# Kernel tuning notes

Measured on AMD Instinct MI355X. Metric: run time of the kernel, lower is better.

The kernel has to match this reference:

```python
import jax, jax.numpy as jnp
import numpy as np
from functools import partial

H = 768
E = 1536
B = 4
L = 4096

def layer_norm(x, g, b, eps=1e-5):
    mu = jnp.mean(x, axis=-1, keepdims=True)
    var = jnp.mean((x - mu) ** 2, axis=-1, keepdims=True)
    return (x - mu) * jax.lax.rsqrt(var + eps) * g + b

def l2_normalize(x, eps=1e-12):
    n = jnp.sqrt(jnp.sum(x * x, axis=-1, keepdims=True))
    return x / jnp.maximum(n, eps)

def dw_conv(x, w):
    # x: [B, L, E], w: [E, 1, 3] depthwise kernel (torch Conv1d groups=E layout)
    y = jax.lax.conv_general_dilated(
        x.transpose(0, 2, 1), w, window_strides=(1,), padding=[(1, 1)],
        dimension_numbers=('NCH', 'OIH', 'NCH'), feature_group_count=E)
    return y.transpose(0, 2, 1)

def setup_inputs() -> dict:
    key = jax.random.key(0)
    ks = jax.random.split(key, 12)
    d = {}
    d['x'] = jax.random.normal(ks[0], (B, L, H), jnp.float32)
    d['ln1_g'] = jnp.ones((H,), jnp.float32)
    d['ln1_b'] = jnp.zeros((H,), jnp.float32)
    d['ln2_g'] = jnp.ones((E,), jnp.float32)
    d['ln2_b'] = jnp.zeros((E,), jnp.float32)
    d['W_in'] = 0.02 * jax.random.normal(ks[1], (3 * E, H), jnp.float32)
    d['b_in'] = jnp.zeros((3 * E,), jnp.float32)
    d['W_beta'] = jnp.zeros((E, H), jnp.float32)  # torch init: constant 0
    d['b_beta'] = jnp.ones((E,), jnp.float32)     # torch init: constant 1
    d['W_out'] = 0.02 * jax.random.normal(ks[2], (H, E), jnp.float32)
    d['b_out'] = jnp.zeros((H,), jnp.float32)
    d['W1'] = 0.02 * jax.random.normal(ks[3], (4 * H, H), jnp.float32)
    d['b1'] = jnp.zeros((4 * H,), jnp.float32)
    d['W2'] = 0.02 * jax.random.normal(ks[4], (H, 4 * H), jnp.float32)
    d['b2'] = jnp.zeros((H,), jnp.float32)
    d['conv_w'] = jax.random.normal(ks[5], (E, 1, 3), jnp.float32) / jnp.sqrt(3.0)
    d['attn_scale'] = jnp.ones((1,), jnp.float32)
    return d

def reference(x, ln1_g, ln1_b, ln2_g, ln2_b, W_in, b_in, W_beta, b_beta,
              W_out, b_out, W1, b1, W2, b2, conv_w, attn_scale):
    shortcut = x
    xn = layer_norm(x, ln1_g, ln1_b)
    qkv = xn @ W_in.T + b_in
    q, k, v = jnp.split(qkv, 3, axis=-1)
    q = jax.nn.silu(q)
    k = jax.nn.silu(k)
    v = jax.nn.gelu(v, approximate=False)
    q = l2_normalize(q) + 0.1 * k
    k = l2_normalize(k) + 0.1 * q
    q = dw_conv(q, conv_w)
    k = dw_conv(k, conv_w)
    v = dw_conv(v, conv_w)
    beta = jax.nn.sigmoid(xn @ W_beta.T + b_beta) * 0.9 + 0.1
    # initial state is zero, so v_old = 0 and v_new = beta * v (same math as torch code)
    v_new = beta * v                                   # [B, L, E]
    state = jnp.einsum('ble,blf->bef', v_new, k)       # v_new^T @ k : [B, E, E]
    out = jnp.einsum('blf,bef->ble', q, state)         # q @ state^T
    out = out * attn_scale
    out = layer_norm(out, ln2_g, ln2_b)
    out = out @ W_out.T + b_out
    x = shortcut + out
    h = layer_norm(x, ln1_g, ln1_b)
    h = jax.nn.gelu(h @ W1.T + b1, approximate=False) @ W2.T + b2
    return x + h
```

## Files before the change

kernel.cpp:

```cpp
#include <hip/hip_runtime.h>
#include <hip/hip_bf16.h>
#include <cstdint>
#include <cstddef>

using bf16_t = __hip_bfloat16;
typedef __bf16 bf16x8 __attribute__((ext_vector_type(8)));
typedef float f32x4 __attribute__((ext_vector_type(4)));

#define DEVI static __device__ __forceinline__

DEVI float b2f(bf16_t v) { return __bfloat162float(v); }
DEVI bf16_t f2b(float v) { return __float2bfloat16(v); }

DEVI float fsigmoid(float x) { return 1.0f / (1.0f + __expf(-x)); }
DEVI float fsilu(float x) { return x * fsigmoid(x); }
DEVI float fgelu(float x) { return 0.5f * x * (1.0f + erff(x * 0.70710678118654752440f)); }

DEVI void g2l16(const bf16_t* g, bf16_t* l) {
    __builtin_amdgcn_global_load_lds(
        (const __attribute__((address_space(1))) void*)g,
        (__attribute__((address_space(3))) void*)l,
        16, 0, 0);
}

template<int ACT, bool RESID, bool OUTBF, bool QKVSPLIT>
__global__ __launch_bounds__(256) void gemm_nt(
    const bf16_t* __restrict__ A, const bf16_t* __restrict__ B,
    void* __restrict__ Cout, const float* __restrict__ bias,
    const float* __restrict__ resid,
    int M, int N, int K, long long sA, long long sB, long long sC)
{
    __shared__ bf16_t As[128 * 32];
    __shared__ bf16_t Bs[128 * 32];

    const int t  = threadIdx.x;
    const int w  = t >> 6;
    const int ln = t & 63;
    const long long bz = blockIdx.z;
    A += bz * sA;
    B += bz * sB;
    const long long cbase = QKVSPLIT ? 0 : bz * sC;

    const int m0 = blockIdx.y * 128;
    const int n0 = blockIdx.x * 128;
    const int wm = (w >> 1) * 64;
    const int wn = (w & 1) * 64;

    f32x4 acc[4][4] = {};

    const int rI0 = (w * 2 + 0) * 16 + (ln >> 2);
    const int rI1 = (w * 2 + 1) * 16 + (ln >> 2);
    const int kc8 = (ln & 3) * 8;
    bf16_t* ldsA0 = &As[(w * 2 + 0) * 512];
    bf16_t* ldsA1 = &As[(w * 2 + 1) * 512];
    bf16_t* ldsB0 = &Bs[(w * 2 + 0) * 512];
    bf16_t* ldsB1 = &Bs[(w * 2 + 1) * 512];

    const int q8 = (ln >> 4) * 8;
    const int fr = ln & 15;

    for (int k0 = 0; k0 < K; k0 += 32) {
        g2l16(A + (size_t)(m0 + rI0) * K + k0 + kc8, ldsA0);
        g2l16(A + (size_t)(m0 + rI1) * K + k0 + kc8, ldsA1);
        g2l16(B + (size_t)(n0 + rI0) * K + k0 + kc8, ldsB0);
        g2l16(B + (size_t)(n0 + rI1) * K + k0 + kc8, ldsB1);
        __syncthreads();

        bf16x8 af[4], bfr[4];
#pragma unroll
        for (int i = 0; i < 4; ++i) {
            af[i]  = *(const bf16x8*)&As[(wm + i * 16 + fr) * 32 + q8];
            bfr[i] = *(const bf16x8*)&Bs[(wn + i * 16 + fr) * 32 + q8];
        }
#pragma unroll
        for (int mi = 0; mi < 4; ++mi)
#pragma unroll
            for (int ni = 0; ni < 4; ++ni)
                acc[mi][ni] = __builtin_amdgcn_mfma_f32_16x16x32_bf16(
                    af[mi], bfr[ni], acc[mi][ni], 0, 0, 0);
        __syncthreads();
    }

    const int rb = (ln >> 4) * 4;
#pragma unroll
    for (int mi = 0; mi < 4; ++mi) {
#pragma unroll
        for (int ni = 0; ni < 4; ++ni) {
            const int col = n0 + wn + ni * 16 + (ln & 15);
            const float bv = bias ? bias[col] : 0.0f;
#pragma unroll
            for (int r = 0; r < 4; ++r) {
                const int row = m0 + wm + mi * 16 + rb + r;
                float v = acc[mi][ni][r] + bv;
                if constexpr (ACT == 1) v = fgelu(v);
                long long off;
                if constexpr (QKVSPLIT) {
                    const int seg = col / 1536;
                    off = (long long)seg * sC + (long long)row * 1536
                        + (col - seg * 1536);
                } else {
                    off = cbase + (long long)row * N + col;
                }
                if constexpr (RESID) v += resid[off];
                if constexpr (OUTBF) ((bf16_t*)Cout)[off] = f2b(v);
                else                 ((float*)Cout)[off] = v;
            }
        }
    }
}

template<int PER>
__global__ __launch_bounds__(256) void ln_fwd(
    const float* __restrict__ x, const float* __restrict__ g,
    const float* __restrict__ b, bf16_t* __restrict__ out,
    const float* __restrict__ scale_ptr)
{
    const int n = PER * 256;
    const int row = blockIdx.x, t = threadIdx.x;
    const float scale = scale_ptr ? scale_ptr[0] : 1.0f;
    const float* xr = x + (size_t)row * n;
    float v[PER];
    float s = 0.f, ss = 0.f;
#pragma unroll
    for (int j = 0; j < PER; ++j) {
        float val = xr[t + 256 * j] * scale;
        v[j] = val; s += val; ss += val * val;
    }
#pragma unroll
    for (int m = 32; m; m >>= 1) { s += __shfl_xor(s, m, 64); ss += __shfl_xor(ss, m, 64); }
    __shared__ float red[8];
    const int w = t >> 6;
    if ((t & 63) == 0) { red[w] = s; red[4 + w] = ss; }
    __syncthreads();
    s  = red[0] + red[1] + red[2] + red[3];
    ss = red[4] + red[5] + red[6] + red[7];
    const float mean = s / n;
    const float var  = ss / n - mean * mean;
    const float rstd = rsqrtf(var + 1e-5f);
    bf16_t* orow = out + (size_t)row * n;
#pragma unroll
    for (int j = 0; j < PER; ++j) {
        const int i = t + 256 * j;
        orow[i] = f2b((v[j] - mean) * rstd * g[i] + b[i]);
    }
}

__global__ __launch_bounds__(256) void qkv_act(bf16_t* __restrict__ qkv, long long SEG)
{
    const int row = blockIdx.x, t = threadIdx.x;
    bf16_t* rq = qkv + (size_t)row * 1536;
    bf16_t* rk = rq + SEG;
    bf16_t* rv = rk + SEG;
    bf16_t* rb = rv + SEG;
    float qv[6], kv[6];
    float sq = 0.f, sk = 0.f;
#pragma unroll
    for (int j = 0; j < 6; ++j) {
        const int i = t + 256 * j;
        float q = fsilu(b2f(rq[i]));
        float k = fsilu(b2f(rk[i]));
        qv[j] = q; kv[j] = k; sq += q * q; sk += k * k;
    }
#pragma unroll
    for (int m = 32; m; m >>= 1) { sq += __shfl_xor(sq, m, 64); sk += __shfl_xor(sk, m, 64); }
    __shared__ float red[8];
    const int w = t >> 6;
    if ((t & 63) == 0) { red[w] = sq; red[4 + w] = sk; }
    __syncthreads();
    sq = red[0] + red[1] + red[2] + red[3];
    sk = red[4] + red[5] + red[6] + red[7];
    const float rqn = 1.0f / fmaxf(sqrtf(sq), 1e-12f);
    const float rkn = 1.0f / fmaxf(sqrtf(sk), 1e-12f);
#pragma unroll
    for (int j = 0; j < 6; ++j) {
        const int i = t + 256 * j;
        const float q1 = qv[j] * rqn + 0.1f * kv[j];
        const float k1 = kv[j] * rkn + 0.1f * q1;
        rq[i] = f2b(q1);
        rk[i] = f2b(k1);
        rv[i] = f2b(fgelu(b2f(rv[i])));
        rb[i] = f2b(fsigmoid(b2f(rb[i])) * 0.9f + 0.1f);
    }
}

template<bool BETA, bool TRANS>
__global__ __launch_bounds__(256) void dwconv(
    const bf16_t* __restrict__ src, const bf16_t* __restrict__ beta,
    bf16_t* __restrict__ dst, const float* __restrict__ cw)
{
    const int L = 4096, E = 1536;
    const int b = blockIdx.z;
    const int e0 = blockIdx.x * 64, l0 = blockIdx.y * 64;
    const int t = threadIdx.x;
    const int el = t & 63, ls = t >> 6;
    const int e = e0 + el;
    const float w0 = cw[e * 3 + 0], w1 = cw[e * 3 + 1], w2 = cw[e * 3 + 2];
    const bf16_t* s = src + (size_t)b * L * E + e;

    __shared__ float Ys[64][65];
#pragma unroll
    for (int j = 0; j < 16; ++j) {
        const int ll = ls + 4 * j;
        const int l = l0 + ll;
        const float xm = (l >= 1)    ? b2f(s[(size_t)(l - 1) * E]) : 0.f;
        const float xc =               b2f(s[(size_t)l * E]);
        const float xp = (l + 1 < L) ? b2f(s[(size_t)(l + 1) * E]) : 0.f;
        float y = w0 * xm + w1 * xc + w2 * xp;
        if constexpr (BETA) y *= b2f(beta[((size_t)b * L + l) * E + e]);
        if constexpr (!TRANS) dst[((size_t)b * L + l) * E + e] = f2b(y);
        else Ys[ll][el] = y;
    }
    if constexpr (TRANS) {
        __syncthreads();
#pragma unroll
        for (int j = 0; j < 16; ++j) {
            const int ew = ls + 4 * j;
            dst[((size_t)b * E + e0 + ew) * L + l0 + el] = f2b(Ys[el][ew]);
        }
    }
}

__global__ __launch_bounds__(256) void cast_f2b(
    const float* __restrict__ src, bf16_t* __restrict__ dst, int n)
{
    const int i = blockIdx.x * 256 + threadIdx.x;
    if (i < n) dst[i] = f2b(src[i]);
}

__global__ void diag_ws(float* o, float v)
{
    o[threadIdx.x] = v;
}


extern "C" void kernel_launch(void* const* d_in, const int* in_sizes, int n_in,
                              void* d_out, int out_size, void* d_ws, size_t ws_size,
                              hipStream_t stream)
{
    constexpr int B = 4, L = 4096, H = 768, E = 1536;
    constexpr int T = B * L;
    constexpr size_t SEGE = (size_t)T * E;
    constexpr size_t S    = SEGE * 2;
    constexpr size_t WS_NEED = 5 * S + 6144 * 4;

    const float* x       = (const float*)d_in[0];
    const float* ln1_g   = (const float*)d_in[1];
    const float* ln1_b   = (const float*)d_in[2];
    const float* ln2_g   = (const float*)d_in[3];
    const float* ln2_b   = (const float*)d_in[4];
    const float* W_in    = (const float*)d_in[5];
    const float* b_in    = (const float*)d_in[6];
    const float* W_beta  = (const float*)d_in[7];
    const float* b_beta  = (const float*)d_in[8];
    const float* W_out   = (const float*)d_in[9];
    const float* b_out   = (const float*)d_in[10];
    const float* W1      = (const float*)d_in[11];
    const float* b1      = (const float*)d_in[12];
    const float* W2      = (const float*)d_in[13];
    const float* b2      = (const float*)d_in[14];
    const float* conv_w  = (const float*)d_in[15];
    const float* attn_sc = (const float*)d_in[16];

    if (ws_size < WS_NEED) {
        diag_ws<<<1, 256, 0, stream>>>((float*)d_out,
                                       10000.0f + (float)(ws_size >> 20));
        return;
    }

    char* ws = (char*)d_ws;
    bf16_t* slotA = (bf16_t*)(ws + 0 * S);
    bf16_t* slotB = (bf16_t*)(ws + 1 * S);
    bf16_t* slotC = (bf16_t*)(ws + 2 * S);
    bf16_t* slotD = (bf16_t*)(ws + 3 * S);
    bf16_t* slotE = (bf16_t*)(ws + 4 * S);
    float*  bcat  = (float*)(ws + 5 * S);

    bf16_t* Wcat = slotE;
    bf16_t* xn   = (bf16_t*)((char*)slotE + (size_t)6144 * H * 2);

    bf16_t* vT    = slotE;
    bf16_t* kT    = slotC;
    bf16_t* qc    = slotD;
    bf16_t* state = slotA;
    float*  attn  = (float*)slotB;
    bf16_t* ln2o  = slotE;
    bf16_t* WoutB = (bf16_t*)((char*)slotB + (size_t)28 * 1024 * 1024);
    bf16_t* W1B   = (bf16_t*)((char*)WoutB + (size_t)H * E * 2);
    bf16_t* W2B   = (bf16_t*)((char*)W1B + (size_t)4 * H * H * 2);
    float*  x2    = (float*)slotA;
    bf16_t* xn2   = slotB;
    bf16_t* h1    = slotC;

    auto cast = [&](const float* s, bf16_t* d, int n) {
        cast_f2b<<<(n + 255) / 256, 256, 0, stream>>>(s, d, n);
    };

    cast(W_in,   Wcat,                     3 * E * H);
    cast(W_beta, Wcat + (size_t)3 * E * H, E * H);
    hipMemcpyAsync(bcat,         b_in,   3 * E * sizeof(float), hipMemcpyDeviceToDevice, stream);
    hipMemcpyAsync(bcat + 3 * E, b_beta, E * sizeof(float),     hipMemcpyDeviceToDevice, stream);

    ln_fwd<3><<<T, 256, 0, stream>>>(x, ln1_g, ln1_b, xn, nullptr);

    gemm_nt<0, false, true, true><<<dim3(6144 / 128, T / 128, 1), 256, 0, stream>>>(
        xn, Wcat, slotA, bcat, nullptr, T, 6144, H, 0, 0, (long long)SEGE);

    qkv_act<<<T, 256, 0, stream>>>(slotA, (long long)SEGE);

    dwconv<true,  true ><<<dim3(E / 64, L / 64, B), 256, 0, stream>>>(slotC, slotD, vT, conv_w);
    dwconv<false, true ><<<dim3(E / 64, L / 64, B), 256, 0, stream>>>(slotB, nullptr, kT, conv_w);
    dwconv<false, false><<<dim3(E / 64, L / 64, B), 256, 0, stream>>>(slotA, nullptr, qc, conv_w);

    gemm_nt<0, false, true, false><<<dim3(E / 128, E / 128, B), 256, 0, stream>>>(
        vT, kT, state, nullptr, nullptr, E, E, L,
        (long long)E * L, (long long)E * L, (long long)E * E);

    gemm_nt<0, false, false, false><<<dim3(E / 128, L / 128, B), 256, 0, stream>>>(
        qc, state, attn, nullptr, nullptr, L, E, E,
        (long long)L * E, (long long)E * E, (long long)L * E);

    ln_fwd<6><<<T, 256, 0, stream>>>(attn, ln2_g, ln2_b, ln2o, attn_sc);

    cast(W_out, WoutB, H * E);
    cast(W1,    W1B,   4 * H * H);
    cast(W2,    W2B,   H * 4 * H);

    gemm_nt<0, true, false, false><<<dim3(H / 128, T / 128, 1), 256, 0, stream>>>(
        ln2o, WoutB, x2, b_out, x, T, H, E, 0, 0, 0);

    ln_fwd<3><<<T, 256, 0, stream>>>(x2, ln1_g, ln1_b, xn2, nullptr);

    gemm_nt<1, false, true, false><<<dim3(4 * H / 128, T / 128, 1), 256, 0, stream>>>(
        xn2, W1B, h1, b1, nullptr, T, 4 * H, H, 0, 0, 0);

    gemm_nt<0, true, false, false><<<dim3(H / 128, T / 128, 1), 256, 0, stream>>>(
        h1, W2B, (float*)d_out, b2, x2, T, H, 4 * H, 0, 0, 0);
}
```

Baseline: 1.234 ms.

## Swizzle GEMM LDS, vectorize epilogues, fuse activations into depthwise conv

The GEMM XOR-swizzles its LDS k-chunks to cut bank conflicts and swaps the MFMA operands so each lane holds four consecutive columns. That lets the epilogue use vector stores for bias, residual and output. LayerNorm and weight casts become float4-vectorized. The qkv activation pass is split into a row-norm kernel plus three act_conv kernels that recompute silu/gelu/sigmoid on the fly inside the depthwise conv with 8-wide loads, which removes the in-place activation write pass. The cost is redundant activation math, since q and k are recomputed in two kernels along with halo rows.

```diff
diff --git a/kernel.cpp b/kernel.cpp
--- a/kernel.cpp
+++ b/kernel.cpp
@@ -5,6 +5,7 @@
 
 using bf16_t = __hip_bfloat16;
 typedef __bf16 bf16x8 __attribute__((ext_vector_type(8)));
+typedef __bf16 bf16x4 __attribute__((ext_vector_type(4)));
 typedef float f32x4 __attribute__((ext_vector_type(4)));
 
 #define DEVI static __device__ __forceinline__
@@ -50,14 +51,14 @@
 
     const int rI0 = (w * 2 + 0) * 16 + (ln >> 2);
     const int rI1 = (w * 2 + 1) * 16 + (ln >> 2);
-    const int kc8 = (ln & 3) * 8;
+    const int kc8 = (((ln & 3) ^ ((ln >> 3) & 3)) * 8);
     bf16_t* ldsA0 = &As[(w * 2 + 0) * 512];
     bf16_t* ldsA1 = &As[(w * 2 + 1) * 512];
     bf16_t* ldsB0 = &Bs[(w * 2 + 0) * 512];
     bf16_t* ldsB1 = &Bs[(w * 2 + 1) * 512];
 
-    const int q8 = (ln >> 4) * 8;
     const int fr = ln & 15;
+    const int koff = (((ln >> 4) ^ ((ln >> 1) & 3)) * 8);
 
     for (int k0 = 0; k0 < K; k0 += 32) {
         g2l16(A + (size_t)(m0 + rI0) * K + k0 + kc8, ldsA0);
@@ -69,168 +70,222 @@
         bf16x8 af[4], bfr[4];
 #pragma unroll
         for (int i = 0; i < 4; ++i) {
-            af[i]  = *(const bf16x8*)&As[(wm + i * 16 + fr) * 32 + q8];
-            bfr[i] = *(const bf16x8*)&Bs[(wn + i * 16 + fr) * 32 + q8];
+            af[i]  = *(const bf16x8*)&As[(wm + i * 16 + fr) * 32 + koff];
+            bfr[i] = *(const bf16x8*)&Bs[(wn + i * 16 + fr) * 32 + koff];
         }
 #pragma unroll
         for (int mi = 0; mi < 4; ++mi)
 #pragma unroll
             for (int ni = 0; ni < 4; ++ni)
                 acc[mi][ni] = __builtin_amdgcn_mfma_f32_16x16x32_bf16(
-                    af[mi], bfr[ni], acc[mi][ni], 0, 0, 0);
+                    bfr[ni], af[mi], acc[mi][ni], 0, 0, 0);
         __syncthreads();
     }
 
     const int rb = (ln >> 4) * 4;
+    f32x4 bias4[4];
+#pragma unroll
+    for (int ni = 0; ni < 4; ++ni) {
+        f32x4 z = {};
+        bias4[ni] = bias ? *(const f32x4*)&bias[n0 + wn + ni * 16 + rb] : z;
+    }
 #pragma unroll
     for (int mi = 0; mi < 4; ++mi) {
+        const int row = m0 + wm + mi * 16 + fr;
 #pragma unroll
         for (int ni = 0; ni < 4; ++ni) {
-            const int col = n0 + wn + ni * 16 + (ln & 15);
-            const float bv = bias ? bias[col] : 0.0f;
-#pragma unroll
-            for (int r = 0; r < 4; ++r) {
-                const int row = m0 + wm + mi * 16 + rb + r;
-                float v = acc[mi][ni][r] + bv;
-                if constexpr (ACT == 1) v = fgelu(v);
-                long long off;
-                if constexpr (QKVSPLIT) {
-                    const int seg = col / 1536;
-                    off = (long long)seg * sC + (long long)row * 1536
-                        + (col - seg * 1536);
-                } else {
-                    off = cbase + (long long)row * N + col;
-                }
-                if constexpr (RESID) v += resid[off];
-                if constexpr (OUTBF) ((bf16_t*)Cout)[off] = f2b(v);
-                else                 ((float*)Cout)[off] = v;
+            const int col0 = n0 + wn + ni * 16 + rb;
+            f32x4 v = acc[mi][ni] + bias4[ni];
+            if constexpr (ACT == 1) {
+#pragma unroll
+                for (int r = 0; r < 4; ++r) v[r] = fgelu(v[r]);
             }
-        }
-    }
-}
-
-template<int PER>
-__global__ __launch_bounds__(256) void ln_fwd(
+            long long off;
+            if constexpr (QKVSPLIT) {
+                const int seg = col0 / 1536;
+                off = (long long)seg * sC + (long long)row * 1536
+                    + (col0 - seg * 1536);
+            } else {
+                off = cbase + (long long)row * N + col0;
+            }
+            if constexpr (RESID) v += *(const f32x4*)&resid[off];
+            if constexpr (OUTBF) {
+                bf16x4 o;
+#pragma unroll
+                for (int r = 0; r < 4; ++r) o[r] = (__bf16)v[r];
+                *(bf16x4*)((bf16_t*)Cout + off) = o;
+            } else {
+                *(f32x4*)((float*)Cout + off) = v;
+            }
+        }
+    }
+}
+
+template<int NT>
+__global__ __launch_bounds__(NT) void ln_v4(
     const float* __restrict__ x, const float* __restrict__ g,
     const float* __restrict__ b, bf16_t* __restrict__ out,
     const float* __restrict__ scale_ptr)
 {
-    const int n = PER * 256;
+    constexpr int n = NT * 4;
+    constexpr int NW = NT / 64;
     const int row = blockIdx.x, t = threadIdx.x;
     const float scale = scale_ptr ? scale_ptr[0] : 1.0f;
-    const float* xr = x + (size_t)row * n;
-    float v[PER];
-    float s = 0.f, ss = 0.f;
-#pragma unroll
-    for (int j = 0; j < PER; ++j) {
-        float val = xr[t + 256 * j] * scale;
-        v[j] = val; s += val; ss += val * val;
-    }
+    f32x4 v = *(const f32x4*)&x[(size_t)row * n + t * 4];
+    v *= scale;
+    float s  = v[0] + v[1] + v[2] + v[3];
+    float ss = v[0]*v[0] + v[1]*v[1] + v[2]*v[2] + v[3]*v[3];
 #pragma unroll
     for (int m = 32; m; m >>= 1) { s += __shfl_xor(s, m, 64); ss += __shfl_xor(ss, m, 64); }
-    __shared__ float red[8];
+    __shared__ float red[2 * NW];
     const int w = t >> 6;
-    if ((t & 63) == 0) { red[w] = s; red[4 + w] = ss; }
+    if ((t & 63) == 0) { red[w] = s; red[NW + w] = ss; }
     __syncthreads();
-    s  = red[0] + red[1] + red[2] + red[3];
-    ss = red[4] + red[5] + red[6] + red[7];
+    s = 0.f; ss = 0.f;
+#pragma unroll
+    for (int i = 0; i < NW; ++i) { s += red[i]; ss += red[NW + i]; }
     const float mean = s / n;
-    const float var  = ss / n - mean * mean;
-    const float rstd = rsqrtf(var + 1e-5f);
-    bf16_t* orow = out + (size_t)row * n;
-#pragma unroll
-    for (int j = 0; j < PER; ++j) {
-        const int i = t + 256 * j;
-        orow[i] = f2b((v[j] - mean) * rstd * g[i] + b[i]);
-    }
-}
-
-__global__ __launch_bounds__(256) void qkv_act(bf16_t* __restrict__ qkv, long long SEG)
+    const float rstd = rsqrtf(ss / n - mean * mean + 1e-5f);
+    const f32x4 gv = *(const f32x4*)&g[t * 4];
+    const f32x4 bv = *(const f32x4*)&b[t * 4];
+    bf16x4 o;
+#pragma unroll
+    for (int r = 0; r < 4; ++r)
+        o[r] = (__bf16)((v[r] - mean) * rstd * gv[r] + bv[r]);
+    *(bf16x4*)&out[(size_t)row * n + t * 4] = o;
+}
+
+__global__ __launch_bounds__(192) void qk_norms(
+    const bf16_t* __restrict__ q, const bf16_t* __restrict__ k,
+    float2* __restrict__ norms)
 {
     const int row = blockIdx.x, t = threadIdx.x;
-    bf16_t* rq = qkv + (size_t)row * 1536;
-    bf16_t* rk = rq + SEG;
-    bf16_t* rv = rk + SEG;
-    bf16_t* rb = rv + SEG;
-    float qv[6], kv[6];
+    const bf16x8 q8 = *(const bf16x8*)&q[(size_t)row * 1536 + t * 8];
+    const bf16x8 k8 = *(const bf16x8*)&k[(size_t)row * 1536 + t * 8];
     float sq = 0.f, sk = 0.f;
 #pragma unroll
-    for (int j = 0; j < 6; ++j) {
-        const int i = t + 256 * j;
-        float q = fsilu(b2f(rq[i]));
-        float k = fsilu(b2f(rk[i]));
-        qv[j] = q; kv[j] = k; sq += q * q; sk += k * k;
+    for (int i = 0; i < 8; ++i) {
+        const float a = fsilu((float)q8[i]);
+        const float c = fsilu((float)k8[i]);
+        sq += a * a; sk += c * c;
     }
 #pragma unroll
     for (int m = 32; m; m >>= 1) { sq += __shfl_xor(sq, m, 64); sk += __shfl_xor(sk, m, 64); }
-    __shared__ float red[8];
+    __shared__ float red[6];
     const int w = t >> 6;
-    if ((t & 63) == 0) { red[w] = sq; red[4 + w] = sk; }
+    if ((t & 63) == 0) { red[w] = sq; red[3 + w] = sk; }
     __syncthreads();
-    sq = red[0] + red[1] + red[2] + red[3];
-    sk = red[4] + red[5] + red[6] + red[7];
-    const float rqn = 1.0f / fmaxf(sqrtf(sq), 1e-12f);
-    const float rkn = 1.0f / fmaxf(sqrtf(sk), 1e-12f);
-#pragma unroll
-    for (int j = 0; j < 6; ++j) {
-        const int i = t + 256 * j;
-        const float q1 = qv[j] * rqn + 0.1f * kv[j];
-        const float k1 = kv[j] * rkn + 0.1f * q1;
-        rq[i] = f2b(q1);
-        rk[i] = f2b(k1);
-        rv[i] = f2b(fgelu(b2f(rv[i])));
-        rb[i] = f2b(fsigmoid(b2f(rb[i])) * 0.9f + 0.1f);
-    }
-}
-
-template<bool BETA, bool TRANS>
-__global__ __launch_bounds__(256) void dwconv(
-    const bf16_t* __restrict__ src, const bf16_t* __restrict__ beta,
+    if (t == 0) {
+        sq = red[0] + red[1] + red[2];
+        sk = red[3] + red[4] + red[5];
+        float2 o;
+        o.x = 1.0f / fmaxf(sqrtf(sq), 1e-12f);
+        o.y = 1.0f / fmaxf(sqrtf(sk), 1e-12f);
+        norms[row] = o;
+    }
+}
+
+template<int STREAM>
+__global__ __launch_bounds__(256) void act_conv(
+    const bf16_t* __restrict__ src0,
+    const bf16_t* __restrict__ src1,
+    const float2* __restrict__ norms,
     bf16_t* __restrict__ dst, const float* __restrict__ cw)
 {
-    const int L = 4096, E = 1536;
+    constexpr int L = 4096, E = 1536;
     const int b = blockIdx.z;
-    const int e0 = blockIdx.x * 64, l0 = blockIdx.y * 64;
+    const int e0 = blockIdx.x * 128, l0 = blockIdx.y * 64;
     const int t = threadIdx.x;
-    const int el = t & 63, ls = t >> 6;
-    const int e = e0 + el;
-    const float w0 = cw[e * 3 + 0], w1 = cw[e * 3 + 1], w2 = cw[e * 3 + 2];
-    const bf16_t* s = src + (size_t)b * L * E + e;
-
-    __shared__ float Ys[64][65];
-#pragma unroll
-    for (int j = 0; j < 16; ++j) {
-        const int ll = ls + 4 * j;
-        const int l = l0 + ll;
-        const float xm = (l >= 1)    ? b2f(s[(size_t)(l - 1) * E]) : 0.f;
-        const float xc =               b2f(s[(size_t)l * E]);
-        const float xp = (l + 1 < L) ? b2f(s[(size_t)(l + 1) * E]) : 0.f;
-        float y = w0 * xm + w1 * xc + w2 * xp;
-        if constexpr (BETA) y *= b2f(beta[((size_t)b * L + l) * E + e]);
-        if constexpr (!TRANS) dst[((size_t)b * L + l) * E + e] = f2b(y);
-        else Ys[ll][el] = y;
-    }
-    if constexpr (TRANS) {
-        __syncthreads();
-#pragma unroll
-        for (int j = 0; j < 16; ++j) {
-            const int ew = ls + 4 * j;
-            dst[((size_t)b * E + e0 + ew) * L + l0 + el] = f2b(Ys[el][ew]);
-        }
-    }
-}
-
-__global__ __launch_bounds__(256) void cast_f2b(
-    const float* __restrict__ src, bf16_t* __restrict__ dst, int n)
+    const int le = t & 15, lt = t >> 4;
+    const int e = e0 + le * 8;
+    const int lbase = l0 + lt * 4;
+    const size_t rowL = (size_t)b * L;
+
+    float w0[8], w1[8], w2[8];
+#pragma unroll
+    for (int i = 0; i < 8; ++i) {
+        w0[i] = cw[(e + i) * 3 + 0];
+        w1[i] = cw[(e + i) * 3 + 1];
+        w2[i] = cw[(e + i) * 3 + 2];
+    }
+
+    float s[6][8];
+#pragma unroll
+    for (int w = 0; w < 6; ++w) {
+        const int l = lbase - 1 + w;
+        if (l < 0 || l >= L) {
+#pragma unroll
+            for (int i = 0; i < 8; ++i) s[w][i] = 0.f;
+            continue;
+        }
+        const size_t off = (rowL + l) * E + e;
+        const bf16x8 a8 = *(const bf16x8*)&src0[off];
+        if constexpr (STREAM == 2) {
+#pragma unroll
+            for (int i = 0; i < 8; ++i) s[w][i] = fgelu((float)a8[i]);
+        } else {
+            const bf16x8 k8 = *(const bf16x8*)&src1[off];
+            const float2 nm = norms[rowL + l];
+#pragma unroll
+            for (int i = 0; i < 8; ++i) {
+                const float sq = fsilu((float)a8[i]);
+                const float sk = fsilu((float)k8[i]);
+                const float q1 = sq * nm.x + 0.1f * sk;
+                s[w][i] = (STREAM == 0) ? q1 : (sk * nm.y + 0.1f * q1);
+            }
+        }
+    }
+
+    float o[4][8];
+#pragma unroll
+    for (int j = 0; j < 4; ++j)
+#pragma unroll
+        for (int i = 0; i < 8; ++i)
+            o[j][i] = w0[i] * s[j][i] + w1[i] * s[j + 1][i] + w2[i] * s[j + 2][i];
+
+    if constexpr (STREAM == 2) {
+#pragma unroll
+        for (int j = 0; j < 4; ++j) {
+            const bf16x8 b8 = *(const bf16x8*)&src1[(rowL + lbase + j) * E + e];
+#pragma unroll
+            for (int i = 0; i < 8; ++i)
+                o[j][i] *= fsigmoid((float)b8[i]) * 0.9f + 0.1f;
+        }
+    }
+
+    if constexpr (STREAM == 0) {
+#pragma unroll
+        for (int j = 0; j < 4; ++j) {
+            bf16x8 ov;
+#pragma unroll
+            for (int i = 0; i < 8; ++i) ov[i] = (__bf16)o[j][i];
+            *(bf16x8*)&dst[(rowL + lbase + j) * E + e] = ov;
+        }
+    } else {
+#pragma unroll
+        for (int i = 0; i < 8; ++i) {
+            bf16x4 ov;
+#pragma unroll
+            for (int j = 0; j < 4; ++j) ov[j] = (__bf16)o[j][i];
+            *(bf16x4*)&dst[((size_t)b * E + e + i) * L + lbase] = ov;
+        }
+    }
+}
+
+__global__ __launch_bounds__(256) void cast_f2b_v4(
+    const float* __restrict__ src, bf16_t* __restrict__ dst, int n4)
 {
     const int i = blockIdx.x * 256 + threadIdx.x;
-    if (i < n) dst[i] = f2b(src[i]);
-}
-
-__global__ void diag_ws(float* o, float v)
-{
-    o[threadIdx.x] = v;
-}
+    if (i < n4) {
+        const f32x4 v = ((const f32x4*)src)[i];
+        bf16x4 o;
+#pragma unroll
+        for (int r = 0; r < 4; ++r) o[r] = (__bf16)v[r];
+        ((bf16x4*)dst)[i] = o;
+    }
+}
+
+__global__ void diag_ws(float* o, float v) { o[threadIdx.x] = v; }
 
 
 extern "C" void kernel_launch(void* const* d_in, const int* in_sizes, int n_in,
@@ -241,7 +296,9 @@
     constexpr int T = B * L;
     constexpr size_t SEGE = (size_t)T * E;
     constexpr size_t S    = SEGE * 2;
-    constexpr size_t WS_NEED = 5 * S + 6144 * 4;
+    constexpr size_t o_bcat  = 5 * S;
+    constexpr size_t o_norms = o_bcat + 6144 * 4;
+    constexpr size_t WS_NEED = o_norms + (size_t)T * 8;
 
     const float* x       = (const float*)d_in[0];
     const float* ln1_g   = (const float*)d_in[1];
@@ -273,7 +330,8 @@
     bf16_t* slotC = (bf16_t*)(ws + 2 * S);
     bf16_t* slotD = (bf16_t*)(ws + 3 * S);
     bf16_t* slotE = (bf16_t*)(ws + 4 * S);
-    float*  bcat  = (float*)(ws + 5 * S);
+    float*  bcat  = (float*)(ws + o_bcat);
+    float2* norms = (float2*)(ws + o_norms);
 
     bf16_t* Wcat = slotE;
     bf16_t* xn   = (bf16_t*)((char*)slotE + (size_t)6144 * H * 2);
@@ -292,7 +350,7 @@
     bf16_t* h1    = slotC;
 
     auto cast = [&](const float* s, bf16_t* d, int n) {
-        cast_f2b<<<(n + 255) / 256, 256, 0, stream>>>(s, d, n);
+        cast_f2b_v4<<<(n / 4 + 255) / 256, 256, 0, stream>>>(s, d, n / 4);
     };
 
     cast(W_in,   Wcat,                     3 * E * H);
@@ -300,16 +358,16 @@
     hipMemcpyAsync(bcat,         b_in,   3 * E * sizeof(float), hipMemcpyDeviceToDevice, stream);
     hipMemcpyAsync(bcat + 3 * E, b_beta, E * sizeof(float),     hipMemcpyDeviceToDevice, stream);
 
-    ln_fwd<3><<<T, 256, 0, stream>>>(x, ln1_g, ln1_b, xn, nullptr);
+    ln_v4<192><<<T, 192, 0, stream>>>(x, ln1_g, ln1_b, xn, nullptr);
 
     gemm_nt<0, false, true, true><<<dim3(6144 / 128, T / 128, 1), 256, 0, stream>>>(
         xn, Wcat, slotA, bcat, nullptr, T, 6144, H, 0, 0, (long long)SEGE);
 
-    qkv_act<<<T, 256, 0, stream>>>(slotA, (long long)SEGE);
-
-    dwconv<true,  true ><<<dim3(E / 64, L / 64, B), 256, 0, stream>>>(slotC, slotD, vT, conv_w);
-    dwconv<false, true ><<<dim3(E / 64, L / 64, B), 256, 0, stream>>>(slotB, nullptr, kT, conv_w);
-    dwconv<false, false><<<dim3(E / 64, L / 64, B), 256, 0, stream>>>(slotA, nullptr, qc, conv_w);
+    qk_norms<<<T, 192, 0, stream>>>(slotA, slotB, norms);
+
+    act_conv<2><<<dim3(E / 128, L / 64, B), 256, 0, stream>>>(slotC, slotD, nullptr, vT, conv_w);
+    act_conv<1><<<dim3(E / 128, L / 64, B), 256, 0, stream>>>(slotA, slotB, norms, kT, conv_w);
+    act_conv<0><<<dim3(E / 128, L / 64, B), 256, 0, stream>>>(slotA, slotB, norms, qc, conv_w);
 
     gemm_nt<0, false, true, false><<<dim3(E / 128, E / 128, B), 256, 0, stream>>>(
         vT, kT, state, nullptr, nullptr, E, E, L,
@@ -319,7 +377,7 @@
         qc, state, attn, nullptr, nullptr, L, E, E,
         (long long)L * E, (long long)E * E, (long long)L * E);
 
-    ln_fwd<6><<<T, 256, 0, stream>>>(attn, ln2_g, ln2_b, ln2o, attn_sc);
+    ln_v4<384><<<T, 384, 0, stream>>>(attn, ln2_g, ln2_b, ln2o, attn_sc);
 
     cast(W_out, WoutB, H * E);
     cast(W1,    W1B,   4 * H * H);
@@ -328,7 +386,7 @@
     gemm_nt<0, true, false, false><<<dim3(H / 128, T / 128, 1), 256, 0, stream>>>(
         ln2o, WoutB, x2, b_out, x, T, H, E, 0, 0, 0);
 
-    ln_fwd<3><<<T, 256, 0, stream>>>(x2, ln1_g, ln1_b, xn2, nullptr);
+    ln_v4<192><<<T, 192, 0, stream>>>(x2, ln1_g, ln1_b, xn2, nullptr);
 
     gemm_nt<1, false, true, false><<<dim3(4 * H / 128, T / 128, 1), 256, 0, stream>>>(
         xn2, W1B, h1, b1, nullptr, T, 4 * H, H, 0, 0, 0);
```

Result: no change. 1.213 ms (-1.7%).
